# Optimization experiments

Hardware: AMD Instinct MI355X
Metric: run time of the kernel (lower is better)

Reference implementation:

```python
import jax, jax.numpy as jnp
import numpy as np

LENGTH_SCALE = 0.1


def setup_inputs() -> dict:
    key = jax.random.key(0)
    k1, k2, k3 = jax.random.split(key, 3)
    features = jax.random.normal(k1, (8, 512, 128, 128), dtype=jnp.float32)
    # nn.Parameter init: normal(0, 0.05)
    weights = jax.random.normal(k2, (16, 64, 512), dtype=jnp.float32) * 0.05
    m = jax.random.normal(k3, (16, 64), dtype=jnp.float32)
    N = jnp.ones((64,), dtype=jnp.float32) * 12.0  # buffer init: ones * 12
    return {"features": features, "weights": weights, "m": m, "N": N}


def reference(features, weights, m, N):
    # per-class linear embedding projection: [b,f,h,w] x [e,c,f] -> [b,e,c,h,w]
    embeddings = jnp.einsum('bfhw,ecf->bechw', features, weights)
    centroids = m / N  # [e, c]
    gamma = -1.0 / (2.0 * LENGTH_SCALE ** 2)
    diff = embeddings - centroids[None, :, :, None, None]
    # squared L2, mean over embedding dim e, RBF exp -> [b, c, h, w]
    out = jnp.exp(jnp.mean(diff * diff, axis=1) * gamma)
    return out
```

## Files before the change

### kernel.cpp

```cpp
#include <hip/hip_runtime.h>

typedef __attribute__((ext_vector_type(8))) short bf16x8;
typedef __attribute__((ext_vector_type(4))) float f32x4;
typedef __attribute__((ext_vector_type(4))) float f4;
typedef __attribute__((ext_vector_type(2))) unsigned int u32x2;
typedef __attribute__((ext_vector_type(4))) unsigned int u32x4;

#define HW   16384
#define FDIM 512

__device__ __forceinline__ unsigned pkhi(float a, float b) {
    return __builtin_amdgcn_perm(__builtin_bit_cast(unsigned int, b),
                                 __builtin_bit_cast(unsigned int, a),
                                 0x07060302u);
}
__device__ __forceinline__ float trhi(float a) {
    return __builtin_bit_cast(float, __builtin_bit_cast(unsigned int, a) & 0xFFFF0000u);
}
__device__ __forceinline__ unsigned pklo(float a, float b) {
    return pkhi(a - trhi(a), b - trhi(b));
}

__global__ __launch_bounds__(256) void conv_w(const float* __restrict__ wts,
                                              unsigned short* __restrict__ wh,
                                              unsigned short* __restrict__ wl) {
    const int tid = blockIdx.x * 256 + threadIdx.x;
    const int n  = tid & 1023;
    const int kc = tid >> 10;
    const float* src = wts + (size_t)((n & 15) * 64 + (n >> 4)) * FDIM + kc * 8;
    f4 a = *(const f4*)src, b = *(const f4*)(src + 4);
    u32x4 h = { pkhi(a[0], a[1]), pkhi(a[2], a[3]), pkhi(b[0], b[1]), pkhi(b[2], b[3]) };
    u32x4 l = { pklo(a[0], a[1]), pklo(a[2], a[3]), pklo(b[0], b[1]), pklo(b[2], b[3]) };
    size_t off = ((size_t)kc * 1024 + n) * 8;
    *(u32x4*)(wh + off) = h;
    *(u32x4*)(wl + off) = l;
}

__global__ __launch_bounds__(256, 4) void duq_main(
    const float* __restrict__ feat,
    const unsigned short* __restrict__ wh,
    const unsigned short* __restrict__ wl,
    const float* __restrict__ m_in,
    const float* __restrict__ n_in,
    float* __restrict__ out)
{
    __shared__ __align__(16) unsigned short Ah[128 * 40];
    __shared__ __align__(16) unsigned short Al[128 * 40];

    const int t  = threadIdx.x;
    const int bx = blockIdx.x;
    const int nb = bx & 7;
    const int mb = bx >> 3;
    const int bidx = mb >> 7;
    const int hw0  = (mb & 127) << 7;

    const int fb = t & 7;
    const int pb = t >> 3;
    const float* ap = feat + (size_t)bidx * (FDIM * HW) + (size_t)(fb * 4) * HW + (hw0 + pb * 4);
    unsigned short* awH = &Ah[(pb * 4) * 40 + fb * 4];
    unsigned short* awL = &Al[(pb * 4) * 40 + fb * 4];

    const int lane = t & 63;
    const int wv = t >> 6;
    const int wm = wv >> 1, wn = wv & 1;
    const int l16 = lane & 15, qd = lane >> 4;

    const unsigned short* arH = &Ah[(wm * 64 + l16) * 40 + qd * 8];
    const unsigned short* arL = &Al[(wm * 64 + l16) * 40 + qd * 8];

    const size_t bgoff = ((size_t)qd * 1024 + (size_t)(nb * 128 + wn * 64 + l16)) * 8;
    const unsigned short* bgh = wh + bgoff;
    const unsigned short* bgl = wl + bgoff;

    f32x4 acc[4][4] = {};

    f4 av[4];
    #pragma unroll
    for (int i = 0; i < 4; ++i) av[i] = *(const f4*)(ap + (size_t)i * HW);

    bf16x8 cbh = *(const bf16x8*)(bgh);
    bf16x8 cbl = *(const bf16x8*)(bgl);
    size_t boff = 0;

    for (int kt = 0; kt < 16; ++kt) {
        __syncthreads();
        #pragma unroll
        for (int j = 0; j < 4; ++j) {
            float a0 = av[0][j], a1 = av[1][j], a2 = av[2][j], a3 = av[3][j];
            u32x2 h, l;
            h[0] = pkhi(a0, a1); h[1] = pkhi(a2, a3);
            l[0] = pklo(a0, a1); l[1] = pklo(a2, a3);
            *(u32x2*)(awH + j * 40) = h;
            *(u32x2*)(awL + j * 40) = l;
        }
        __syncthreads();

        if (kt < 15) {
            ap += 32 * HW;
            #pragma unroll
            for (int i = 0; i < 4; ++i) av[i] = *(const f4*)(ap + (size_t)i * HW);
        }

        bf16x8 fah[4], fal[4];
        #pragma unroll
        for (int i = 0; i < 4; ++i) {
            fah[i] = *(const bf16x8*)(arH + i * 640);
            fal[i] = *(const bf16x8*)(arL + i * 640);
        }

        #pragma unroll
        for (int j = 0; j < 4; ++j) {
            size_t bnext = boff + ((j == 3) ? (size_t)(32768 - 384) : (size_t)128);
            bf16x8 nbh = *(const bf16x8*)(bgh + bnext);
            bf16x8 nbl = *(const bf16x8*)(bgl + bnext);
            #pragma unroll
            for (int i = 0; i < 4; ++i) {
                acc[i][j] = __builtin_amdgcn_mfma_f32_16x16x32_bf16(fah[i], cbh, acc[i][j], 0, 0, 0);
                acc[i][j] = __builtin_amdgcn_mfma_f32_16x16x32_bf16(fah[i], cbl, acc[i][j], 0, 0, 0);
                acc[i][j] = __builtin_amdgcn_mfma_f32_16x16x32_bf16(fal[i], cbh, acc[i][j], 0, 0, 0);
            }
            cbh = nbh; cbl = nbl; boff = bnext;
        }
    }

    float centv[4];
    #pragma unroll
    for (int j = 0; j < 4; ++j) {
        int cj = nb * 8 + wn * 4 + j;
        centv[j] = m_in[l16 * 64 + cj] / n_in[cj];
    }
    #pragma unroll
    for (int i = 0; i < 4; ++i) {
        #pragma unroll
        for (int j = 0; j < 4; ++j) {
            float s0 = acc[i][j][0] - centv[j]; s0 *= s0;
            float s1 = acc[i][j][1] - centv[j]; s1 *= s1;
            float s2 = acc[i][j][2] - centv[j]; s2 *= s2;
            float s3 = acc[i][j][3] - centv[j]; s3 *= s3;
            #pragma unroll
            for (int msk = 1; msk < 16; msk <<= 1) {
                s0 += __shfl_xor(s0, msk, 64);
                s1 += __shfl_xor(s1, msk, 64);
                s2 += __shfl_xor(s2, msk, 64);
                s3 += __shfl_xor(s3, msk, 64);
            }
            if (l16 == 0) {
                int cj = nb * 8 + wn * 4 + j;
                f4 o;
                o[0] = __expf(s0 * -3.125f);
                o[1] = __expf(s1 * -3.125f);
                o[2] = __expf(s2 * -3.125f);
                o[3] = __expf(s3 * -3.125f);
                size_t off = ((size_t)(bidx * 64 + cj)) * HW
                           + (size_t)(hw0 + wm * 64 + i * 16 + qd * 4);
                *(f4*)(out + off) = o;
            }
        }
    }
}

__global__ __launch_bounds__(256) void duq_fallback(
    const float* __restrict__ feat, const float* __restrict__ wts,
    const float* __restrict__ m_in, const float* __restrict__ n_in,
    float* __restrict__ out)
{
    __shared__ __align__(16) unsigned short Ah[128 * 40];
    __shared__ __align__(16) unsigned short Al[128 * 40];
    __shared__ __align__(16) unsigned short Bh[128 * 40];
    __shared__ __align__(16) unsigned short Bl[128 * 40];

    const int t  = threadIdx.x;
    const int bx = blockIdx.x;
    const int nb = bx & 7;
    const int mb = bx >> 3;
    const int bidx = mb >> 7;
    const int hw0  = (mb & 127) << 7;

    const int fb = t & 7;
    const int pb = t >> 3;
    const float* ap = feat + (size_t)bidx * (FDIM * HW) + (size_t)(fb * 4) * HW + (hw0 + pb * 4);

    const int bn  = t >> 1;
    const int bh_ = t & 1;
    const int ng  = nb * 128 + bn;
    const float* bp = wts + (size_t)((ng & 15) * 64 + (ng >> 4)) * FDIM + bh_ * 16;

    unsigned short* awH = &Ah[(pb * 4) * 40 + fb * 4];
    unsigned short* awL = &Al[(pb * 4) * 40 + fb * 4];
    unsigned short* bwH = &Bh[bn * 40 + bh_ * 16];
    unsigned short* bwL = &Bl[bn * 40 + bh_ * 16];

    const int lane = t & 63;
    const int wv = t >> 6;
    const int wm = wv >> 1, wn = wv & 1;
    const int l16 = lane & 15, qd = lane >> 4;

    const unsigned short* arH = &Ah[(wm * 64 + l16) * 40 + qd * 8];
    const unsigned short* arL = &Al[(wm * 64 + l16) * 40 + qd * 8];
    const unsigned short* brH = &Bh[(wn * 64 + l16) * 40 + qd * 8];
    const unsigned short* brL = &Bl[(wn * 64 + l16) * 40 + qd * 8];

    f32x4 acc[4][4] = {};

    f4 av[4], bv[4];
    #pragma unroll
    for (int i = 0; i < 4; ++i) av[i] = *(const f4*)(ap + (size_t)i * HW);
    #pragma unroll
    for (int q = 0; q < 4; ++q) bv[q] = *(const f4*)(bp + q * 4);

    for (int kt = 0; kt < 16; ++kt) {
        __syncthreads();
        #pragma unroll
        for (int j = 0; j < 4; ++j) {
            float a0 = av[0][j], a1 = av[1][j], a2 = av[2][j], a3 = av[3][j];
            u32x2 h, l;
            h[0] = pkhi(a0, a1); h[1] = pkhi(a2, a3);
            l[0] = pklo(a0, a1); l[1] = pklo(a2, a3);
            *(u32x2*)(awH + j * 40) = h;
            *(u32x2*)(awL + j * 40) = l;
        }
        {
            u32x4 h0 = { pkhi(bv[0][0], bv[0][1]), pkhi(bv[0][2], bv[0][3]),
                         pkhi(bv[1][0], bv[1][1]), pkhi(bv[1][2], bv[1][3]) };
            u32x4 h1 = { pkhi(bv[2][0], bv[2][1]), pkhi(bv[2][2], bv[2][3]),
                         pkhi(bv[3][0], bv[3][1]), pkhi(bv[3][2], bv[3][3]) };
            u32x4 l0 = { pklo(bv[0][0], bv[0][1]), pklo(bv[0][2], bv[0][3]),
                         pklo(bv[1][0], bv[1][1]), pklo(bv[1][2], bv[1][3]) };
            u32x4 l1 = { pklo(bv[2][0], bv[2][1]), pklo(bv[2][2], bv[2][3]),
                         pklo(bv[3][0], bv[3][1]), pklo(bv[3][2], bv[3][3]) };
            *(u32x4*)(bwH)     = h0;  *(u32x4*)(bwH + 8) = h1;
            *(u32x4*)(bwL)     = l0;  *(u32x4*)(bwL + 8) = l1;
        }
        __syncthreads();

        if (kt < 15) {
            ap += 32 * HW;
            bp += 32;
            #pragma unroll
            for (int i = 0; i < 4; ++i) av[i] = *(const f4*)(ap + (size_t)i * HW);
            #pragma unroll
            for (int q = 0; q < 4; ++q) bv[q] = *(const f4*)(bp + q * 4);
        }

        bf16x8 fah[4], fal[4];
        #pragma unroll
        for (int i = 0; i < 4; ++i) {
            fah[i] = *(const bf16x8*)(arH + i * 640);
            fal[i] = *(const bf16x8*)(arL + i * 640);
        }
        #pragma unroll
        for (int j = 0; j < 4; ++j) {
            bf16x8 fbh = *(const bf16x8*)(brH + j * 640);
            bf16x8 fbl = *(const bf16x8*)(brL + j * 640);
            #pragma unroll
            for (int i = 0; i < 4; ++i) {
                acc[i][j] = __builtin_amdgcn_mfma_f32_16x16x32_bf16(fah[i], fbh, acc[i][j], 0, 0, 0);
                acc[i][j] = __builtin_amdgcn_mfma_f32_16x16x32_bf16(fah[i], fbl, acc[i][j], 0, 0, 0);
                acc[i][j] = __builtin_amdgcn_mfma_f32_16x16x32_bf16(fal[i], fbh, acc[i][j], 0, 0, 0);
            }
        }
    }

    float centv[4];
    #pragma unroll
    for (int j = 0; j < 4; ++j) {
        int cj = nb * 8 + wn * 4 + j;
        centv[j] = m_in[l16 * 64 + cj] / n_in[cj];
    }
    #pragma unroll
    for (int i = 0; i < 4; ++i) {
        #pragma unroll
        for (int j = 0; j < 4; ++j) {
            float s0 = acc[i][j][0] - centv[j]; s0 *= s0;
            float s1 = acc[i][j][1] - centv[j]; s1 *= s1;
            float s2 = acc[i][j][2] - centv[j]; s2 *= s2;
            float s3 = acc[i][j][3] - centv[j]; s3 *= s3;
            #pragma unroll
            for (int msk = 1; msk < 16; msk <<= 1) {
                s0 += __shfl_xor(s0, msk, 64);
                s1 += __shfl_xor(s1, msk, 64);
                s2 += __shfl_xor(s2, msk, 64);
                s3 += __shfl_xor(s3, msk, 64);
            }
            if (l16 == 0) {
                int cj = nb * 8 + wn * 4 + j;
                f4 o;
                o[0] = __expf(s0 * -3.125f);
                o[1] = __expf(s1 * -3.125f);
                o[2] = __expf(s2 * -3.125f);
                o[3] = __expf(s3 * -3.125f);
                size_t off = ((size_t)(bidx * 64 + cj)) * HW
                           + (size_t)(hw0 + wm * 64 + i * 16 + qd * 4);
                *(f4*)(out + off) = o;
            }
        }
    }
}

extern "C" void kernel_launch(void* const* d_in, const int* in_sizes, int n_in,
                              void* d_out, int out_size, void* d_ws, size_t ws_size,
                              hipStream_t stream) {
    const float* feat = (const float*)d_in[0];
    const float* wts  = (const float*)d_in[1];
    const float* mbuf = (const float*)d_in[2];
    const float* nbuf = (const float*)d_in[3];
    float* out = (float*)d_out;

    if (ws_size >= (size_t)(2 * 1024 * 1024 + 128 * 1024)) {
        unsigned short* wh = (unsigned short*)d_ws;
        unsigned short* wl = wh + 512 * 1024;
        conv_w<<<dim3(256), dim3(256), 0, stream>>>(wts, wh, wl);
        duq_main<<<dim3(1024 * 8), dim3(256), 0, stream>>>(feat, wh, wl, mbuf, nbuf, out);
    } else {
        duq_fallback<<<dim3(1024 * 8), dim3(256), 0, stream>>>(feat, wts, mbuf, nbuf, out);
    }
}
```

Before: 718.8 us.

## Double-buffer LDS A tiles, remap block order, and raise MFMA priority

Splits the shared-memory A tile into two buffers so the next K-slice is converted and written while the current one is consumed, leaving one barrier per iteration instead of two. The block index mapping now puts the 8 N-blocks of one M tile on far-apart block IDs, with consecutive blocks walking different M tiles, which changes L2 reuse of the feature data. It also wraps the MFMA section in s_setprio. LDS use doubles, which may cut occupancy from the 4 blocks per CU set in launch_bounds.

```diff
diff --git a/kernel.cpp b/kernel.cpp
--- a/kernel.cpp
+++ b/kernel.cpp
@@ -44,29 +44,27 @@
     const float* __restrict__ n_in,
     float* __restrict__ out)
 {
-    __shared__ __align__(16) unsigned short Ah[128 * 40];
-    __shared__ __align__(16) unsigned short Al[128 * 40];
+    __shared__ __align__(16) unsigned short Ah[2][128 * 40];
+    __shared__ __align__(16) unsigned short Al[2][128 * 40];
 
     const int t  = threadIdx.x;
     const int bx = blockIdx.x;
-    const int nb = bx & 7;
-    const int mb = bx >> 3;
+    const int kb = bx >> 3;
+    const int nb = kb & 7;
+    const int mb = (bx & 7) * 128 + (kb >> 3);
     const int bidx = mb >> 7;
     const int hw0  = (mb & 127) << 7;
 
     const int fb = t & 7;
     const int pb = t >> 3;
     const float* ap = feat + (size_t)bidx * (FDIM * HW) + (size_t)(fb * 4) * HW + (hw0 + pb * 4);
-    unsigned short* awH = &Ah[(pb * 4) * 40 + fb * 4];
-    unsigned short* awL = &Al[(pb * 4) * 40 + fb * 4];
+    const int aw = (pb * 4) * 40 + fb * 4;
 
     const int lane = t & 63;
     const int wv = t >> 6;
     const int wm = wv >> 1, wn = wv & 1;
     const int l16 = lane & 15, qd = lane >> 4;
-
-    const unsigned short* arH = &Ah[(wm * 64 + l16) * 40 + qd * 8];
-    const unsigned short* arL = &Al[(wm * 64 + l16) * 40 + qd * 8];
+    const int ar = (wm * 64 + l16) * 40 + qd * 8;
 
     const size_t bgoff = ((size_t)qd * 1024 + (size_t)(nb * 128 + wn * 64 + l16)) * 8;
     const unsigned short* bgh = wh + bgoff;
@@ -78,22 +76,24 @@
     #pragma unroll
     for (int i = 0; i < 4; ++i) av[i] = *(const f4*)(ap + (size_t)i * HW);
 
+    #pragma unroll
+    for (int j = 0; j < 4; ++j) {
+        float a0 = av[0][j], a1 = av[1][j], a2 = av[2][j], a3 = av[3][j];
+        u32x2 h, l;
+        h[0] = pkhi(a0, a1); h[1] = pkhi(a2, a3);
+        l[0] = pklo(a0, a1); l[1] = pklo(a2, a3);
+        *(u32x2*)(&Ah[0][aw + j * 40]) = h;
+        *(u32x2*)(&Al[0][aw + j * 40]) = l;
+    }
+
     bf16x8 cbh = *(const bf16x8*)(bgh);
     bf16x8 cbl = *(const bf16x8*)(bgl);
     size_t boff = 0;
 
+    __syncthreads();
+
     for (int kt = 0; kt < 16; ++kt) {
-        __syncthreads();
-        #pragma unroll
-        for (int j = 0; j < 4; ++j) {
-            float a0 = av[0][j], a1 = av[1][j], a2 = av[2][j], a3 = av[3][j];
-            u32x2 h, l;
-            h[0] = pkhi(a0, a1); h[1] = pkhi(a2, a3);
-            l[0] = pklo(a0, a1); l[1] = pklo(a2, a3);
-            *(u32x2*)(awH + j * 40) = h;
-            *(u32x2*)(awL + j * 40) = l;
-        }
-        __syncthreads();
+        const int cur = kt & 1;
 
         if (kt < 15) {
             ap += 32 * HW;
@@ -104,10 +104,11 @@
         bf16x8 fah[4], fal[4];
         #pragma unroll
         for (int i = 0; i < 4; ++i) {
-            fah[i] = *(const bf16x8*)(arH + i * 640);
-            fal[i] = *(const bf16x8*)(arL + i * 640);
-        }
-
+            fah[i] = *(const bf16x8*)(&Ah[cur][ar + i * 640]);
+            fal[i] = *(const bf16x8*)(&Al[cur][ar + i * 640]);
+        }
+
+        __builtin_amdgcn_s_setprio(1);
         #pragma unroll
         for (int j = 0; j < 4; ++j) {
             size_t bnext = boff + ((j == 3) ? (size_t)(32768 - 384) : (size_t)128);
@@ -120,6 +121,21 @@
                 acc[i][j] = __builtin_amdgcn_mfma_f32_16x16x32_bf16(fal[i], cbh, acc[i][j], 0, 0, 0);
             }
             cbh = nbh; cbl = nbl; boff = bnext;
+        }
+        __builtin_amdgcn_s_setprio(0);
+
+        if (kt < 15) {
+            const int nxtb = cur ^ 1;
+            #pragma unroll
+            for (int j = 0; j < 4; ++j) {
+                float a0 = av[0][j], a1 = av[1][j], a2 = av[2][j], a3 = av[3][j];
+                u32x2 h, l;
+                h[0] = pkhi(a0, a1); h[1] = pkhi(a2, a3);
+                l[0] = pklo(a0, a1); l[1] = pklo(a2, a3);
+                *(u32x2*)(&Ah[nxtb][aw + j * 40]) = h;
+                *(u32x2*)(&Al[nxtb][aw + j * 40]) = l;
+            }
+            __syncthreads();
         }
     }
 
```

Result: slower. 1.171 ms (+62.9%).
